# Kernel tuning notes

Hardware: AMD Instinct MI355X
Metric: run time of the kernel (lower is better)

The kernel has to match this reference:

```python
import jax, jax.numpy as jnp
import numpy as np

B, L, K, I, O = 4, 10000, 16, 256, 256


def setup_inputs() -> dict:
    key = jax.random.key(0)
    k1, k2, k3 = jax.random.split(key, 3)
    x = jax.random.normal(k1, (B, L, I), dtype=jnp.float32)
    index_tensor = jax.random.randint(k2, (L, K), 0, L, dtype=jnp.int64)
    stdv = 0.5
    mask = jax.random.uniform(k3, (K, I, O), dtype=jnp.float32, minval=-stdv, maxval=stdv)
    bias = jnp.zeros((O,), dtype=jnp.float32)
    return {"x": x, "index_tensor": index_tensor, "mask": mask, "bias": bias}


def reference(x, index_tensor, mask, bias):
    # torch: expand x to [b,l,l,i], gather along dim2 with index[l,k] -> [b,l,k,i]
    # equivalent: per output node n, neighbors x[:, index_tensor[n, j], :]
    gathered = x[:, index_tensor, :]            # [b, l, k, i]
    # flatten(k,i) @ flatten(mask: [k*i, o]) == einsum over k,i
    y = jnp.einsum('blki,kio->blo', gathered, mask) + bias
    return y
```

## Files before the change

kernel.cpp:

```cpp
#include <hip/hip_runtime.h>

#define Bdim 4
#define Ldim 10000
#define Kdim 16
#define Idim 256
#define Odim 256

typedef __attribute__((ext_vector_type(8))) __bf16 bf16x8;
typedef __attribute__((ext_vector_type(4))) float f32x4;

__global__ __launch_bounds__(256)
void prepack(const float* __restrict__ x, const float* __restrict__ mask,
             __bf16* __restrict__ xb, __bf16* __restrict__ wpk)
{
    const int b = blockIdx.x;
    if (b < 2500) {
        const size_t base = ((size_t)b * 256 + threadIdx.x) * 16;
#pragma unroll
        for (int j = 0; j < 2; ++j) {
            const float4 f0 = *(const float4*)(x + base + j * 8);
            const float4 f1 = *(const float4*)(x + base + j * 8 + 4);
            bf16x8 v;
            v[0] = (__bf16)f0.x; v[1] = (__bf16)f0.y; v[2] = (__bf16)f0.z; v[3] = (__bf16)f0.w;
            v[4] = (__bf16)f1.x; v[5] = (__bf16)f1.y; v[6] = (__bf16)f1.z; v[7] = (__bf16)f1.w;
            *(bf16x8*)(xb + base + j * 8) = v;
        }
    } else {
        const int tg = (b - 2500) * 256 + threadIdx.x;
        const int c  = tg >> 6;
        const int ln = tg & 63;
        const int ni  = c & 3;
        const int ks  = (c >> 2) & 1;
        const int wid = (c >> 3) & 3;
        const int kb  = c >> 5;
        const int n   = wid * 64 + ni * 16 + (ln & 15);
        const int kk0 = kb * 64 + ks * 32 + (ln >> 4) * 8;
        bf16x8 v;
#pragma unroll
        for (int j = 0; j < 8; ++j)
            v[j] = (__bf16)mask[(size_t)(kk0 + j) * Odim + n];
        *(bf16x8*)(wpk + (size_t)tg * 8) = v;
    }
}

#define TL 16
#define BM 64
#define LDA 72

__global__ __launch_bounds__(256, 3)
void piconv_gemm(const __bf16* __restrict__ xb,
                 const int* __restrict__ idxT,
                 const __bf16* __restrict__ wpk,
                 const float* __restrict__ bias,
                 float* __restrict__ out)
{
    __shared__ __bf16 Alds[2][BM * LDA];
    __shared__ int    idx_lds[TL * Kdim];

    const int t    = threadIdx.x;
    const int l0   = blockIdx.x * TL;
    const int lane = t & 63;
    const int wid  = t >> 6;
    const int q    = lane >> 4;
    const int r16  = lane & 15;

    idx_lds[t] = idxT[l0 * Kdim + t];

    const int arow  = t >> 2;
    const int apart = t & 3;
    const int alt   = arow & 15;
    const int abb   = arow >> 4;
    const size_t abase = ((size_t)abb * Ldim) << 8;

    const __bf16* wbase = wpk + ((size_t)(wid * 8) << 9) + lane * 8;

    f32x4  acc[4][4] = {};
    bf16x8 aN0, aN1, wA[8], wB[8];

    __syncthreads();

    {
        const int iv = idx_lds[alt * Kdim];
        const __bf16* s = xb + abase + (((size_t)iv) << 8) + apart * 16;
        aN0 = *(const bf16x8*)s;
        aN1 = *(const bf16x8*)(s + 8);
#pragma unroll
        for (int j = 0; j < 8; ++j)
            wA[j] = *(const bf16x8*)(wbase + j * 512);
    }

#define STEP(KB, BUF, WCUR, WNXT, PF)                                           \
    {                                                                           \
        *(bf16x8*)&Alds[BUF][arow * LDA + apart * 16]     = aN0;                \
        *(bf16x8*)&Alds[BUF][arow * LDA + apart * 16 + 8] = aN1;                \
        __syncthreads();                                                        \
        if (PF) {                                                               \
            const int kn = ((KB) + 1) >> 2;                                     \
            const int io = ((((KB) + 1) & 3) << 6) + apart * 16;                \
            const int iv = idx_lds[alt * Kdim + kn];                            \
            const __bf16* s = xb + abase + (((size_t)iv) << 8) + io;            \
            aN0 = *(const bf16x8*)s;                                            \
            aN1 = *(const bf16x8*)(s + 8);                                      \
            const __bf16* wq = wbase + ((size_t)((KB) + 1)) * 16384;            \
            _Pragma("unroll")                                                   \
            for (int j = 0; j < 8; ++j)                                         \
                WNXT[j] = *(const bf16x8*)(wq + j * 512);                       \
        }                                                                       \
        _Pragma("unroll")                                                       \
        for (int ks = 0; ks < 2; ++ks) {                                        \
            bf16x8 af[4];                                                       \
            _Pragma("unroll")                                                   \
            for (int mi = 0; mi < 4; ++mi)                                      \
                af[mi] = *(bf16x8*)&Alds[BUF][(mi * 16 + r16) * LDA + ks * 32 + q * 8]; \
            _Pragma("unroll")                                                   \
            for (int mi = 0; mi < 4; ++mi)                                      \
                _Pragma("unroll")                                               \
                for (int ni = 0; ni < 4; ++ni)                                  \
                    acc[mi][ni] = __builtin_amdgcn_mfma_f32_16x16x32_bf16(      \
                        af[mi], WCUR[ks * 4 + ni], acc[mi][ni], 0, 0, 0);       \
        }                                                                       \
    }

    for (int kb2 = 0; kb2 < 32; ++kb2) {
        STEP(2 * kb2,     0, wA, wB, true)
        STEP(2 * kb2 + 1, 1, wB, wA, (2 * kb2 + 1) < 63)
    }
#undef STEP

    float bv[4];
#pragma unroll
    for (int ni = 0; ni < 4; ++ni)
        bv[ni] = bias[wid * 64 + ni * 16 + r16];
#pragma unroll
    for (int mi = 0; mi < 4; ++mi) {
#pragma unroll
        for (int rr = 0; rr < 4; ++rr) {
            const int lt = q * 4 + rr;
            float* dst = out + (((size_t)(mi * Ldim + l0 + lt)) << 8) + wid * 64 + r16;
#pragma unroll
            for (int ni = 0; ni < 4; ++ni)
                dst[ni * 16] = acc[mi][ni][rr] + bv[ni];
        }
    }
}

#define FTL 32
#define FBN 128
#define FLDA 72
__global__ __launch_bounds__(256)
void piconv_fallback(const float* __restrict__ x,
                     const int* __restrict__ idxT,
                     const float* __restrict__ mask,
                     const float* __restrict__ bias,
                     float* __restrict__ out)
{
    __shared__ __bf16 Alds[128 * FLDA];
    __shared__ __bf16 Wlds[FBN * FLDA];
    const int t  = threadIdx.x;
    const int l0 = blockIdx.x * FTL;
    const int n0 = blockIdx.y * FBN;
    const int lane = t & 63;
    const int wid  = t >> 6;
    const int wm   = wid >> 1;
    const int wn   = wid & 1;
    const int q    = lane >> 4;
    const int r16  = lane & 15;
    f32x4 acc[4][4] = {};
    const int am    = t >> 1;
    const int ahalf = t & 1;
    const int alt   = am & 31;
    const int abb   = am >> 5;
    const int al    = l0 + alt;
    const bool avalid = (al < Ldim);
    for (int kb = 0; kb < 64; ++kb) {
        {
            const int ksl = kb >> 2;
            const int i0  = ((kb & 3) << 6) + (ahalf << 5);
            const int idx = avalid ? idxT[al * Kdim + ksl] : 0;
            const float* src = x + (((size_t)(abb * Ldim + idx)) << 8) + i0;
#pragma unroll
            for (int j = 0; j < 4; ++j) {
                const float4 f0 = *(const float4*)(src + j * 8);
                const float4 f1 = *(const float4*)(src + j * 8 + 4);
                bf16x8 v;
                v[0] = (__bf16)f0.x; v[1] = (__bf16)f0.y; v[2] = (__bf16)f0.z; v[3] = (__bf16)f0.w;
                v[4] = (__bf16)f1.x; v[5] = (__bf16)f1.y; v[6] = (__bf16)f1.z; v[7] = (__bf16)f1.w;
                *(bf16x8*)&Alds[am * FLDA + (ahalf << 5) + j * 8] = v;
            }
        }
        {
#pragma unroll
            for (int it = 0; it < 4; ++it) {
                const int pair = t + it * 256;
                const int n    = pair & 127;
                const int g    = pair >> 7;
                const float* src = mask + (((size_t)(kb * 64 + g * 8)) << 8) + n0 + n;
                bf16x8 v;
#pragma unroll
                for (int j = 0; j < 8; ++j)
                    v[j] = (__bf16)src[(size_t)j << 8];
                *(bf16x8*)&Wlds[n * FLDA + g * 8] = v;
            }
        }
        __syncthreads();
#pragma unroll
        for (int ks = 0; ks < 2; ++ks) {
            bf16x8 af[4], bfr[4];
#pragma unroll
            for (int mi = 0; mi < 4; ++mi)
                af[mi] = *(bf16x8*)&Alds[(wm * 64 + mi * 16 + r16) * FLDA + ks * 32 + q * 8];
#pragma unroll
            for (int ni = 0; ni < 4; ++ni)
                bfr[ni] = *(bf16x8*)&Wlds[(wn * 64 + ni * 16 + r16) * FLDA + ks * 32 + q * 8];
#pragma unroll
            for (int mi = 0; mi < 4; ++mi)
#pragma unroll
                for (int ni = 0; ni < 4; ++ni)
                    acc[mi][ni] = __builtin_amdgcn_mfma_f32_16x16x32_bf16(
                        af[mi], bfr[ni], acc[mi][ni], 0, 0, 0);
        }
        __syncthreads();
    }
    float bv[4];
#pragma unroll
    for (int ni = 0; ni < 4; ++ni)
        bv[ni] = bias[n0 + wn * 64 + ni * 16 + r16];
#pragma unroll
    for (int mi = 0; mi < 4; ++mi) {
        const int mrow = wm * 64 + mi * 16 + q * 4;
#pragma unroll
        for (int rr = 0; rr < 4; ++rr) {
            const int m  = mrow + rr;
            const int lt = m & 31;
            const int bb = m >> 5;
            const int l  = l0 + lt;
            if (l < Ldim) {
                float* dst = out + (((size_t)(bb * Ldim + l)) << 8) + n0 + wn * 64 + r16;
#pragma unroll
                for (int ni = 0; ni < 4; ++ni)
                    dst[ni * 16] = acc[mi][ni][rr] + bv[ni];
            }
        }
    }
}

extern "C" void kernel_launch(void* const* d_in, const int* in_sizes, int n_in,
                              void* d_out, int out_size, void* d_ws, size_t ws_size,
                              hipStream_t stream) {
    const float* x    = (const float*)d_in[0];
    const int*   idx  = (const int*)d_in[1];
    const float* mask = (const float*)d_in[2];
    const float* bias = (const float*)d_in[3];
    float* out = (float*)d_out;

    const size_t xb_bytes = (size_t)Bdim * Ldim * Idim * 2;
    const size_t wp_bytes = (size_t)Kdim * Idim * Odim * 2;

    if (ws_size >= xb_bytes + wp_bytes) {
        __bf16* xb  = (__bf16*)d_ws;
        __bf16* wpk = (__bf16*)((char*)d_ws + xb_bytes);
        prepack<<<2500 + 512, 256, 0, stream>>>(x, mask, xb, wpk);
        piconv_gemm<<<Ldim / TL, 256, 0, stream>>>(xb, idx, wpk, bias, out);
    } else {
        dim3 grid((Ldim + FTL - 1) / FTL, Odim / FBN, 1);
        piconv_fallback<<<grid, 256, 0, stream>>>(x, idx, mask, bias, out);
    }
}
```

Baseline: 187.8 us.

## Split GEMM reduction over K into two blocks with atomic accumulation

Splits the 64-step reduction across two grid slices along blockIdx.y, giving each block half of the neighbor indices, and combines the partial sums with float atomic adds into an output that prepack now zeroes. The goal is twice as many blocks (1250 instead of 625) to fill the GPU's compute units and hide latency. In exchange it adds a 41 MB zeroing pass and atomic read-modify-write traffic on the output, and summation order becomes nondeterministic.

After: 226.2 us. 20.4% more time.

```diff
diff --git a/kernel.cpp b/kernel.cpp
--- a/kernel.cpp
+++ b/kernel.cpp
@@ -11,7 +11,8 @@
 
 __global__ __launch_bounds__(256)
 void prepack(const float* __restrict__ x, const float* __restrict__ mask,
-             __bf16* __restrict__ xb, __bf16* __restrict__ wpk)
+             __bf16* __restrict__ xb, __bf16* __restrict__ wpk,
+             float* __restrict__ out)
 {
     const int b = blockIdx.x;
     if (b < 2500) {
@@ -25,7 +26,7 @@
             v[4] = (__bf16)f1.x; v[5] = (__bf16)f1.y; v[6] = (__bf16)f1.z; v[7] = (__bf16)f1.w;
             *(bf16x8*)(xb + base + j * 8) = v;
         }
-    } else {
+    } else if (b < 3012) {
         const int tg = (b - 2500) * 256 + threadIdx.x;
         const int c  = tg >> 6;
         const int ln = tg & 63;
@@ -40,6 +41,9 @@
         for (int j = 0; j < 8; ++j)
             v[j] = (__bf16)mask[(size_t)(kk0 + j) * Odim + n];
         *(bf16x8*)(wpk + (size_t)tg * 8) = v;
+    } else {
+        const size_t o = ((size_t)(b - 3012) * 256 + threadIdx.x) * 4;
+        *(float4*)(out + o) = float4{0.f, 0.f, 0.f, 0.f};
     }
 }
 
@@ -55,16 +59,21 @@
                  float* __restrict__ out)
 {
     __shared__ __bf16 Alds[2][BM * LDA];
-    __shared__ int    idx_lds[TL * Kdim];
+    __shared__ int    idx_lds[TL * 8];
 
     const int t    = threadIdx.x;
     const int l0   = blockIdx.x * TL;
+    const int z    = blockIdx.y;
+    const int kb0  = z * 32;
     const int lane = t & 63;
     const int wid  = t >> 6;
     const int q    = lane >> 4;
     const int r16  = lane & 15;
 
-    idx_lds[t] = idxT[l0 * Kdim + t];
+    if (t < TL * 8) {
+        const int lt = t >> 3, kl = t & 7;
+        idx_lds[t] = idxT[(l0 + lt) * Kdim + z * 8 + kl];
+    }
 
     const int arow  = t >> 2;
     const int apart = t & 3;
@@ -80,13 +89,14 @@
     __syncthreads();
 
     {
-        const int iv = idx_lds[alt * Kdim];
+        const int iv = idx_lds[alt * 8];
         const __bf16* s = xb + abase + (((size_t)iv) << 8) + apart * 16;
         aN0 = *(const bf16x8*)s;
         aN1 = *(const bf16x8*)(s + 8);
+        const __bf16* wq = wbase + (size_t)kb0 * 16384;
 #pragma unroll
         for (int j = 0; j < 8; ++j)
-            wA[j] = *(const bf16x8*)(wbase + j * 512);
+            wA[j] = *(const bf16x8*)(wq + j * 512);
     }
 
 #define STEP(KB, BUF, WCUR, WNXT, PF)                                           \
@@ -95,9 +105,9 @@
         *(bf16x8*)&Alds[BUF][arow * LDA + apart * 16 + 8] = aN1;                \
         __syncthreads();                                                        \
         if (PF) {                                                               \
-            const int kn = ((KB) + 1) >> 2;                                     \
+            const int kl = (((KB) + 1) >> 2) - (kb0 >> 2);                      \
             const int io = ((((KB) + 1) & 3) << 6) + apart * 16;                \
-            const int iv = idx_lds[alt * Kdim + kn];                            \
+            const int iv = idx_lds[alt * 8 + kl];                               \
             const __bf16* s = xb + abase + (((size_t)iv) << 8) + io;            \
             aN0 = *(const bf16x8*)s;                                            \
             aN1 = *(const bf16x8*)(s + 8);                                      \
@@ -121,16 +131,17 @@
         }                                                                       \
     }
 
-    for (int kb2 = 0; kb2 < 32; ++kb2) {
-        STEP(2 * kb2,     0, wA, wB, true)
-        STEP(2 * kb2 + 1, 1, wB, wA, (2 * kb2 + 1) < 63)
+    for (int s2 = 0; s2 < 16; ++s2) {
+        const int kb = kb0 + 2 * s2;
+        STEP(kb,     0, wA, wB, true)
+        STEP(kb + 1, 1, wB, wA, (2 * s2 + 1) < 31)
     }
 #undef STEP
 
     float bv[4];
 #pragma unroll
     for (int ni = 0; ni < 4; ++ni)
-        bv[ni] = bias[wid * 64 + ni * 16 + r16];
+        bv[ni] = (z == 0) ? bias[wid * 64 + ni * 16 + r16] : 0.0f;
 #pragma unroll
     for (int mi = 0; mi < 4; ++mi) {
 #pragma unroll
@@ -139,7 +150,7 @@
             float* dst = out + (((size_t)(mi * Ldim + l0 + lt)) << 8) + wid * 64 + r16;
 #pragma unroll
             for (int ni = 0; ni < 4; ++ni)
-                dst[ni * 16] = acc[mi][ni][rr] + bv[ni];
+                unsafeAtomicAdd(dst + ni * 16, acc[mi][ni][rr] + bv[ni]);
         }
     }
 }
@@ -259,8 +270,8 @@
     if (ws_size >= xb_bytes + wp_bytes) {
         __bf16* xb  = (__bf16*)d_ws;
         __bf16* wpk = (__bf16*)((char*)d_ws + xb_bytes);
-        prepack<<<2500 + 512, 256, 0, stream>>>(x, mask, xb, wpk);
-        piconv_gemm<<<Ldim / TL, 256, 0, stream>>>(xb, idx, wpk, bias, out);
+        prepack<<<2500 + 512 + 10000, 256, 0, stream>>>(x, mask, xb, wpk, out);
+        piconv_gemm<<<dim3(Ldim / TL, 2), 256, 0, stream>>>(xb, idx, wpk, bias, out);
     } else {
         dim3 grid((Ldim + FTL - 1) / FTL, Odim / FBN, 1);
         piconv_fallback<<<grid, 256, 0, stream>>>(x, idx, mask, bias, out);
```

## Load gathered A fragments directly from global into registers, dropping LDS staging

Applied to the files above, without the earlier changes.

Each wave now gathers its own MFMA A-operand fragments straight from global memory into double-buffered registers, replacing the shared-memory tile and the per-step barrier. This removes the LDS writes, LDS reads and __syncthreads in the K loop. The cost is that every one of the four waves loads the same A data (4x redundant global/L2 traffic), register pressure rises from the extra fragment buffers, and the occupancy hint in launch bounds is dropped.

Result: slower. 318.7 us (+69.7%).

```diff
diff --git a/kernel.cpp b/kernel.cpp
--- a/kernel.cpp
+++ b/kernel.cpp
@@ -44,18 +44,15 @@
 }
 
 #define TL 16
-#define BM 64
-#define LDA 72
-
-__global__ __launch_bounds__(256, 3)
+
+__global__ __launch_bounds__(256)
 void piconv_gemm(const __bf16* __restrict__ xb,
                  const int* __restrict__ idxT,
                  const __bf16* __restrict__ wpk,
                  const float* __restrict__ bias,
                  float* __restrict__ out)
 {
-    __shared__ __bf16 Alds[2][BM * LDA];
-    __shared__ int    idx_lds[TL * Kdim];
+    __shared__ int idx_lds[TL * Kdim];
 
     const int t    = threadIdx.x;
     const int l0   = blockIdx.x * TL;
@@ -66,64 +63,57 @@
 
     idx_lds[t] = idxT[l0 * Kdim + t];
 
-    const int arow  = t >> 2;
-    const int apart = t & 3;
-    const int alt   = arow & 15;
-    const int abb   = arow >> 4;
-    const size_t abase = ((size_t)abb * Ldim) << 8;
-
     const __bf16* wbase = wpk + ((size_t)(wid * 8) << 9) + lane * 8;
 
     f32x4  acc[4][4] = {};
-    bf16x8 aN0, aN1, wA[8], wB[8];
+    bf16x8 aA[8], aB[8], wA[8], wB[8];
 
     __syncthreads();
 
     {
-        const int iv = idx_lds[alt * Kdim];
-        const __bf16* s = xb + abase + (((size_t)iv) << 8) + apart * 16;
-        aN0 = *(const bf16x8*)s;
-        aN1 = *(const bf16x8*)(s + 8);
+        const int iv = idx_lds[r16 * Kdim];
+        const __bf16* s = xb + ((size_t)iv << 8) + q * 8;
+#pragma unroll
+        for (int mi = 0; mi < 4; ++mi) {
+            const __bf16* sm = s + (size_t)mi * (Ldim * 256);
+            aA[mi]     = *(const bf16x8*)sm;
+            aA[4 + mi] = *(const bf16x8*)(sm + 32);
+        }
 #pragma unroll
         for (int j = 0; j < 8; ++j)
             wA[j] = *(const bf16x8*)(wbase + j * 512);
     }
 
-#define STEP(KB, BUF, WCUR, WNXT, PF)                                           \
+#define STEP(KB, ACUR, ANXT, WCUR, WNXT, PF)                                    \
     {                                                                           \
-        *(bf16x8*)&Alds[BUF][arow * LDA + apart * 16]     = aN0;                \
-        *(bf16x8*)&Alds[BUF][arow * LDA + apart * 16 + 8] = aN1;                \
-        __syncthreads();                                                        \
         if (PF) {                                                               \
-            const int kn = ((KB) + 1) >> 2;                                     \
-            const int io = ((((KB) + 1) & 3) << 6) + apart * 16;                \
-            const int iv = idx_lds[alt * Kdim + kn];                            \
-            const __bf16* s = xb + abase + (((size_t)iv) << 8) + io;            \
-            aN0 = *(const bf16x8*)s;                                            \
-            aN1 = *(const bf16x8*)(s + 8);                                      \
-            const __bf16* wq = wbase + ((size_t)((KB) + 1)) * 16384;            \
+            const int kbn = (KB) + 1;                                           \
+            const int iv  = idx_lds[r16 * Kdim + (kbn >> 2)];                   \
+            const __bf16* s = xb + ((size_t)iv << 8) + ((kbn & 3) << 6) + q * 8;\
+            _Pragma("unroll")                                                   \
+            for (int mi = 0; mi < 4; ++mi) {                                    \
+                const __bf16* sm = s + (size_t)mi * (Ldim * 256);               \
+                ANXT[mi]     = *(const bf16x8*)sm;                              \
+                ANXT[4 + mi] = *(const bf16x8*)(sm + 32);                       \
+            }                                                                   \
+            const __bf16* wq = wbase + (size_t)kbn * 16384;                     \
             _Pragma("unroll")                                                   \
             for (int j = 0; j < 8; ++j)                                         \
                 WNXT[j] = *(const bf16x8*)(wq + j * 512);                       \
         }                                                                       \
         _Pragma("unroll")                                                       \
-        for (int ks = 0; ks < 2; ++ks) {                                        \
-            bf16x8 af[4];                                                       \
-            _Pragma("unroll")                                                   \
-            for (int mi = 0; mi < 4; ++mi)                                      \
-                af[mi] = *(bf16x8*)&Alds[BUF][(mi * 16 + r16) * LDA + ks * 32 + q * 8]; \
+        for (int ks = 0; ks < 2; ++ks)                                          \
             _Pragma("unroll")                                                   \
             for (int mi = 0; mi < 4; ++mi)                                      \
                 _Pragma("unroll")                                               \
                 for (int ni = 0; ni < 4; ++ni)                                  \
                     acc[mi][ni] = __builtin_amdgcn_mfma_f32_16x16x32_bf16(      \
-                        af[mi], WCUR[ks * 4 + ni], acc[mi][ni], 0, 0, 0);       \
-        }                                                                       \
+                        ACUR[ks * 4 + mi], WCUR[ks * 4 + ni], acc[mi][ni], 0, 0, 0); \
     }
 
     for (int kb2 = 0; kb2 < 32; ++kb2) {
-        STEP(2 * kb2,     0, wA, wB, true)
-        STEP(2 * kb2 + 1, 1, wB, wA, (2 * kb2 + 1) < 63)
+        STEP(2 * kb2,     aA, aB, wA, wB, true)
+        STEP(2 * kb2 + 1, aB, aA, wB, wA, (2 * kb2 + 1) < 63)
     }
 #undef STEP
 
```
